# Performance work log

Measured on AMD Instinct MI355X. Metric: run time of the kernel, lower is better.

The kernel has to match this reference:

```python
import jax, jax.numpy as jnp
import numpy as np

C, W, H = 16, 48, 48
OUTDIMS = 4000
COMPONENTS = 1
BATCH = 128
EPS = 1e-6
INIT_NOISE = 1e-3


def setup_inputs() -> dict:
    key = jax.random.key(0)
    kx, kw, kh, kf = jax.random.split(key, 4)
    x = jax.random.normal(kx, (BATCH, C, W, H), dtype=jnp.float32)
    width = jax.random.normal(kw, (OUTDIMS, 1, W, 1, COMPONENTS), dtype=jnp.float32) * INIT_NOISE
    height = jax.random.normal(kh, (OUTDIMS, 1, 1, H, COMPONENTS), dtype=jnp.float32) * INIT_NOISE
    features = jax.random.normal(kf, (OUTDIMS, C, 1, 1), dtype=jnp.float32) * INIT_NOISE
    bias = jnp.zeros((OUTDIMS,), dtype=jnp.float32)
    return {"x": x, "width": width, "height": height, "features": features, "bias": bias}


def reference(x, width, height, features, bias):
    # normalize width over the w axis (dim 2), height over the h axis (dim 3)
    wn = width / jnp.sqrt(jnp.sum(width * width, axis=2, keepdims=True) + EPS)
    hn = height / jnp.sqrt(jnp.sum(height * height, axis=3, keepdims=True) + EPS)
    # spatial mask: sum of outer products over components -> (outdims, w, h)
    spatial = jnp.sum(wn * hn, axis=4)[:, 0]  # broadcast (n,1,w,1,k)*(n,1,1,h,k)
    feat = features[:, :, 0, 0]  # (outdims, c)
    # y[b,n] = sum_{c,w,h} x[b,c,w,h] * spatial[n,w,h] * feat[n,c]  (same math as
    # x.view(N,-1) @ weight.t() where weight = spatial * features, flattened cwh)
    y = jnp.einsum('bcwh,nwh,nc->bn', x, spatial, feat)
    return y + bias[None, :]
```

## Files before the change

kernel.cpp:

```cpp
#include <hip/hip_runtime.h>
#include <stdint.h>

#define OUTD 4000
#define NPAD 4096
#define CC 16
#define WW 48
#define HH 48
#define BB 128
#define KD 768
#define MD 6144
#define EPSF 1e-6f

#define BM 192
#define BNB 256
#define BKU 64
#define UNITS 12
#define AELEMS (BM * BKU)
#define BELEMS (BNB * BKU)
#define SLOTE (AELEMS + BELEMS)
#define THREADS 512
#define XPB 2304

using short8 = __attribute__((ext_vector_type(8))) short;
using f32x4  = __attribute__((ext_vector_type(4))) float;

static __device__ __forceinline__ unsigned short f2bf(float f) {
  union { float f; unsigned int u; } v; v.f = f;
  unsigned int u = v.u;
  unsigned int r = (u + 0x7FFFu + ((u >> 16) & 1u)) >> 16;
  return (unsigned short)r;
}

__global__ __launch_bounds__(256)
void prep_all(const float* __restrict__ x,
              const float* __restrict__ width,
              const float* __restrict__ height,
              const float* __restrict__ feat,
              unsigned short* __restrict__ A,
              unsigned short* __restrict__ Qt,
              float* __restrict__ wnT) {
  __shared__ float smw[4][WW];
  int bid = blockIdx.x;
  if (bid < XPB) {
    int t = bid * 256 + threadIdx.x;
    int e = t * 8;
    int h0 = e % HH;
    int w = (e / HH) % WW;
    int c = (e / (HH * WW)) % CC;
    int b = e / (HH * WW * CC);
    float4 v0 = *(const float4*)(x + e);
    float4 v1 = *(const float4*)(x + e + 4);
    short8 o;
    o[0] = (short)f2bf(v0.x); o[1] = (short)f2bf(v0.y);
    o[2] = (short)f2bf(v0.z); o[3] = (short)f2bf(v0.w);
    o[4] = (short)f2bf(v1.x); o[5] = (short)f2bf(v1.y);
    o[6] = (short)f2bf(v1.z); o[7] = (short)f2bf(v1.w);
    *(short8*)&A[(size_t)(b * WW + w) * KD + c * HH + h0] = o;
  } else {
    int lane = threadIdx.x & 63;
    int wv = threadIdx.x >> 6;
    int nbase = (bid - XPB) * 4;
    int n = nbase + wv;
    bool valid = (n < OUTD);
    float hv = (valid && lane < HH) ? height[n * HH + lane] : 0.f;
    float wvv = (valid && lane < WW) ? width[n * WW + lane] : 0.f;
    float hs = hv * hv, wsum = wvv * wvv;
    #pragma unroll
    for (int off = 32; off > 0; off >>= 1) {
      hs += __shfl_xor(hs, off);
      wsum += __shfl_xor(wsum, off);
    }
    float hnorm = rsqrtf(hs + EPSF);
    float wnorm = rsqrtf(wsum + EPSF);
    if (lane < WW) smw[wv][lane] = wvv * wnorm;
    if (valid) {
      #pragma unroll
      for (int i = lane; i < KD; i += 64) {
        int c = i / HH, h = i % HH;
        Qt[(size_t)n * KD + i] = f2bf(feat[n * CC + c] * height[n * HH + h] * hnorm);
      }
    } else {
      #pragma unroll
      for (int i = lane; i < KD; i += 64) Qt[(size_t)n * KD + i] = 0;
    }
    __syncthreads();
    if (threadIdx.x < WW) {
      int w = threadIdx.x;
      float4 o = make_float4(smw[0][w], smw[1][w], smw[2][w], smw[3][w]);
      *(float4*)&wnT[w * NPAD + nbase] = o;
    }
  }
}

__global__ __launch_bounds__(THREADS, 2)
void gemm_main(const unsigned short* __restrict__ A,
               const unsigned short* __restrict__ Qt,
               const float* __restrict__ wnT,
               const float* __restrict__ bias,
               float* __restrict__ out) {
  __shared__ unsigned short S[2 * SLOTE];

  int tid = threadIdx.x;
  int lane = tid & 63;
  int wid = tid >> 6;
  int wm = wid >> 2;
  int wn = wid & 3;

  int bid = blockIdx.x;
  int xcd = bid & 7;
  int i = bid >> 3;
  int by = xcd * 4 + (i & 3);
  int bxg = i >> 2;
  int n0 = bxg * BNB;
  int m0 = by * BM;

  int rsub = lane >> 3;
  int cg = lane & 7;
  int gsw = (cg ^ rsub) * 8;
  const unsigned short* gA[3];
  const unsigned short* gB[4];
  #pragma unroll
  for (int j = 0; j < 3; ++j)
    gA[j] = A + (size_t)(m0 + (wid * 3 + j) * 8 + rsub) * KD + gsw;
  #pragma unroll
  for (int j = 0; j < 4; ++j)
    gB[j] = Qt + (size_t)(n0 + (wid * 4 + j) * 8 + rsub) * KD + gsw;
  int aD[3], bD[4];
  #pragma unroll
  for (int j = 0; j < 3; ++j) aD[j] = (wid * 3 + j) * 512;
  #pragma unroll
  for (int j = 0; j < 4; ++j) bD[j] = AELEMS + (wid * 4 + j) * 512;

#define SLOTB(u) (((u) & 1) * SLOTE)
#define STAGE(u)                                                                    \
  { _Pragma("unroll")                                                               \
    for (int j = 0; j < 3; ++j)                                                     \
      __builtin_amdgcn_global_load_lds(                                             \
          (const __attribute__((address_space(1))) void*)(gA[j] + (u) * BKU),       \
          (__attribute__((address_space(3))) void*)(&S[SLOTB(u) + aD[j]]), 16, 0, 0); \
    _Pragma("unroll")                                                               \
    for (int j = 0; j < 4; ++j)                                                     \
      __builtin_amdgcn_global_load_lds(                                             \
          (const __attribute__((address_space(1))) void*)(gB[j] + (u) * BKU),       \
          (__attribute__((address_space(3))) void*)(&S[SLOTB(u) + bD[j]]), 16, 0, 0); }

  int q16 = lane & 15;
  int hi = lane >> 4;
  int q7 = q16 & 7;
  int kg0 = ((0 * 4 + hi) ^ q7) * 8;
  int kg1 = ((1 * 4 + hi) ^ q7) * 8;
  int arow = (wm * 96 + q16) * BKU;
  int brow = AELEMS + (wn * 64 + q16) * BKU;

  f32x4 acc[6][4] = {};
  short8 afA[6], bfA[4], afB[6], bfB[4];

#define DSREAD_H(afX, bfX, u, kg)                                      \
  { const unsigned short* sb = &S[SLOTB(u)];                           \
    _Pragma("unroll")                                                  \
    for (int mi = 0; mi < 6; ++mi)                                     \
      afX[mi] = *(const short8*)&sb[arow + mi * 16 * BKU + (kg)];      \
    _Pragma("unroll")                                                  \
    for (int ni = 0; ni < 4; ++ni)                                     \
      bfX[ni] = *(const short8*)&sb[brow + ni * 16 * BKU + (kg)]; }

#define MFMA24(afX, bfX)                                               \
  { _Pragma("unroll")                                                  \
    for (int ni = 0; ni < 4; ++ni)                                     \
      _Pragma("unroll")                                                \
      for (int mi = 0; mi < 6; ++mi)                                   \
        acc[mi][ni] = __builtin_amdgcn_mfma_f32_16x16x32_bf16(afX[mi], bfX[ni], acc[mi][ni], 0, 0, 0); }

  STAGE(0);

  #pragma unroll
  for (int u = 0; u < UNITS; ++u) {
    if (u + 1 < UNITS) {
      STAGE(u + 1);
      asm volatile("s_waitcnt vmcnt(7)" ::: "memory");
    } else {
      asm volatile("s_waitcnt vmcnt(0)" ::: "memory");
    }
    __builtin_amdgcn_s_barrier();
    __builtin_amdgcn_sched_barrier(0);

    DSREAD_H(afA, bfA, u, kg0);
    asm volatile("s_waitcnt lgkmcnt(0)" ::: "memory");
    __builtin_amdgcn_sched_barrier(0);
    DSREAD_H(afB, bfB, u, kg1);
    __builtin_amdgcn_s_setprio(1);
    MFMA24(afA, bfA);
    asm volatile("s_waitcnt lgkmcnt(0)" ::: "memory");
    __builtin_amdgcn_sched_barrier(0);
    MFMA24(afB, bfB);
    __builtin_amdgcn_s_setprio(0);
    __builtin_amdgcn_sched_barrier(0);
  }

  int b0 = by * 4 + wm * 2;
  #pragma unroll
  for (int ni = 0; ni < 4; ++ni) {
    int ng = n0 + wn * 64 + ni * 16 + q16;
    float s0 = 0.f, s1 = 0.f;
    #pragma unroll
    for (int mi = 0; mi < 3; ++mi) {
      int wbase = mi * 16 + hi * 4;
      f32x4 va = acc[mi][ni];
      f32x4 vb = acc[mi + 3][ni];
      #pragma unroll
      for (int r = 0; r < 4; ++r) {
        float t = wnT[(wbase + r) * NPAD + ng];
        s0 += t * va[r];
        s1 += t * vb[r];
      }
    }
    s0 += __shfl_xor(s0, 16); s0 += __shfl_xor(s0, 32);
    s1 += __shfl_xor(s1, 16); s1 += __shfl_xor(s1, 32);
    if (hi == 0 && ng < OUTD) {
      float bv = bias[ng];
      out[(size_t)b0 * OUTD + ng] = s0 + bv;
      out[(size_t)(b0 + 1) * OUTD + ng] = s1 + bv;
    }
  }
#undef STAGE
#undef SLOTB
#undef DSREAD_H
#undef MFMA24
}

extern "C" void kernel_launch(void* const* d_in, const int* in_sizes, int n_in,
                              void* d_out, int out_size, void* d_ws, size_t ws_size,
                              hipStream_t stream) {
  const float* x      = (const float*)d_in[0];
  const float* width  = (const float*)d_in[1];
  const float* height = (const float*)d_in[2];
  const float* feat   = (const float*)d_in[3];
  const float* bias   = (const float*)d_in[4];
  float* out = (float*)d_out;

  char* ws = (char*)d_ws;
  unsigned short* A  = (unsigned short*)ws;
  unsigned short* Qt = (unsigned short*)(ws + 9437184);
  float* wnT         = (float*)(ws + 9437184 + 6291456);

  prep_all<<<dim3(XPB + NPAD / 4), dim3(256), 0, stream>>>(x, width, height, feat, A, Qt, wnT);
  gemm_main<<<dim3(512), dim3(THREADS), 0, stream>>>(A, Qt, wnT, bias, out);
}
```

Before: 48.90 us.

## Use 4 waves with larger per-wave N tile and halve K step

New measurement: 54.68 us. +11.8%, slower.

```diff
diff --git a/kernel.cpp b/kernel.cpp
--- a/kernel.cpp
+++ b/kernel.cpp
@@ -13,12 +13,11 @@
 
 #define BM 192
 #define BNB 256
-#define BKU 64
-#define UNITS 12
+#define BKU 32
+#define UNITS 24
 #define AELEMS (BM * BKU)
-#define BELEMS (BNB * BKU)
-#define SLOTE (AELEMS + BELEMS)
-#define THREADS 512
+#define SLOT_ELEMS ((BM + BNB) * BKU)
+#define THREADS 256
 #define XPB 2304
 
 using short8 = __attribute__((ext_vector_type(8))) short;
@@ -98,13 +97,13 @@
                const float* __restrict__ wnT,
                const float* __restrict__ bias,
                float* __restrict__ out) {
-  __shared__ unsigned short S[2 * SLOTE];
+  __shared__ unsigned short S[2 * SLOT_ELEMS];
 
   int tid = threadIdx.x;
   int lane = tid & 63;
   int wid = tid >> 6;
-  int wm = wid >> 2;
-  int wn = wid & 3;
+  int wm = wid >> 1;
+  int wn = wid & 1;
 
   int bid = blockIdx.x;
   int xcd = bid & 7;
@@ -114,62 +113,41 @@
   int n0 = bxg * BNB;
   int m0 = by * BM;
 
-  int rsub = lane >> 3;
-  int cg = lane & 7;
-  int gsw = (cg ^ rsub) * 8;
-  const unsigned short* gA[3];
-  const unsigned short* gB[4];
-  #pragma unroll
-  for (int j = 0; j < 3; ++j)
-    gA[j] = A + (size_t)(m0 + (wid * 3 + j) * 8 + rsub) * KD + gsw;
-  #pragma unroll
-  for (int j = 0; j < 4; ++j)
-    gB[j] = Qt + (size_t)(n0 + (wid * 4 + j) * 8 + rsub) * KD + gsw;
-  int aD[3], bD[4];
-  #pragma unroll
-  for (int j = 0; j < 3; ++j) aD[j] = (wid * 3 + j) * 512;
-  #pragma unroll
-  for (int j = 0; j < 4; ++j) bD[j] = AELEMS + (wid * 4 + j) * 512;
-
-#define SLOTB(u) (((u) & 1) * SLOTE)
-#define STAGE(u)                                                                    \
-  { _Pragma("unroll")                                                               \
-    for (int j = 0; j < 3; ++j)                                                     \
-      __builtin_amdgcn_global_load_lds(                                             \
-          (const __attribute__((address_space(1))) void*)(gA[j] + (u) * BKU),       \
-          (__attribute__((address_space(3))) void*)(&S[SLOTB(u) + aD[j]]), 16, 0, 0); \
-    _Pragma("unroll")                                                               \
-    for (int j = 0; j < 4; ++j)                                                     \
-      __builtin_amdgcn_global_load_lds(                                             \
-          (const __attribute__((address_space(1))) void*)(gB[j] + (u) * BKU),       \
-          (__attribute__((address_space(3))) void*)(&S[SLOTB(u) + bD[j]]), 16, 0, 0); }
+  int lrow = lane >> 2;
+  int g = lane & 3;
+  int gsw = (g ^ ((lrow >> 1) & 3)) * 8;
+  const unsigned short* gsrc[7];
+  int ldst[7];
+  #pragma unroll
+  for (int j = 0; j < 3; ++j) {
+    int c = wid * 3 + j;
+    gsrc[j] = A + (size_t)(m0 + c * 16 + lrow) * KD + gsw;
+    ldst[j] = c * 512;
+  }
+  #pragma unroll
+  for (int j = 0; j < 4; ++j) {
+    int c = wid * 4 + j;
+    gsrc[3 + j] = Qt + (size_t)(n0 + c * 16 + lrow) * KD + gsw;
+    ldst[3 + j] = AELEMS + c * 512;
+  }
+
+#define SLOTB(u) (((u) & 1) * SLOT_ELEMS)
+#define STAGE(u)                                                                  \
+  { _Pragma("unroll")                                                             \
+    for (int j = 0; j < 7; ++j)                                                   \
+      __builtin_amdgcn_global_load_lds(                                           \
+          (const __attribute__((address_space(1))) void*)(gsrc[j] + (u) * BKU),   \
+          (__attribute__((address_space(3))) void*)(&S[SLOTB(u) + ldst[j]]), 16, 0, 0); }
 
   int q16 = lane & 15;
   int hi = lane >> 4;
-  int q7 = q16 & 7;
-  int kg0 = ((0 * 4 + hi) ^ q7) * 8;
-  int kg1 = ((1 * 4 + hi) ^ q7) * 8;
-  int arow = (wm * 96 + q16) * BKU;
-  int brow = AELEMS + (wn * 64 + q16) * BKU;
-
-  f32x4 acc[6][4] = {};
-  short8 afA[6], bfA[4], afB[6], bfB[4];
-
-#define DSREAD_H(afX, bfX, u, kg)                                      \
-  { const unsigned short* sb = &S[SLOTB(u)];                           \
-    _Pragma("unroll")                                                  \
-    for (int mi = 0; mi < 6; ++mi)                                     \
-      afX[mi] = *(const short8*)&sb[arow + mi * 16 * BKU + (kg)];      \
-    _Pragma("unroll")                                                  \
-    for (int ni = 0; ni < 4; ++ni)                                     \
-      bfX[ni] = *(const short8*)&sb[brow + ni * 16 * BKU + (kg)]; }
-
-#define MFMA24(afX, bfX)                                               \
-  { _Pragma("unroll")                                                  \
-    for (int ni = 0; ni < 4; ++ni)                                     \
-      _Pragma("unroll")                                                \
-      for (int mi = 0; mi < 6; ++mi)                                   \
-        acc[mi][ni] = __builtin_amdgcn_mfma_f32_16x16x32_bf16(afX[mi], bfX[ni], acc[mi][ni], 0, 0, 0); }
+  int kgr = (hi ^ ((q16 >> 1) & 3)) * 8;
+  int arow = (wm * 96 + q16) * BKU + kgr;
+  int brow = AELEMS + (wn * 128 + q16) * BKU + kgr;
+
+  f32x4 acc[6][8] = {};
+  short8 af[6];
+  short8 bf[4];
 
   STAGE(0);
 
@@ -184,23 +162,41 @@
     __builtin_amdgcn_s_barrier();
     __builtin_amdgcn_sched_barrier(0);
 
-    DSREAD_H(afA, bfA, u, kg0);
+    const unsigned short* sb = &S[SLOTB(u)];
+    #pragma unroll
+    for (int mi = 0; mi < 6; ++mi)
+      af[mi] = *(const short8*)&sb[arow + mi * 512];
+    #pragma unroll
+    for (int ni = 0; ni < 4; ++ni)
+      bf[ni] = *(const short8*)&sb[brow + ni * 512];
     asm volatile("s_waitcnt lgkmcnt(0)" ::: "memory");
     __builtin_amdgcn_sched_barrier(0);
-    DSREAD_H(afB, bfB, u, kg1);
     __builtin_amdgcn_s_setprio(1);
-    MFMA24(afA, bfA);
+    #pragma unroll
+    for (int ni = 0; ni < 4; ++ni)
+      #pragma unroll
+      for (int mi = 0; mi < 6; ++mi)
+        acc[mi][ni] = __builtin_amdgcn_mfma_f32_16x16x32_bf16(af[mi], bf[ni], acc[mi][ni], 0, 0, 0);
+    __builtin_amdgcn_s_setprio(0);
+    #pragma unroll
+    for (int ni = 0; ni < 4; ++ni)
+      bf[ni] = *(const short8*)&sb[brow + (4 + ni) * 512];
     asm volatile("s_waitcnt lgkmcnt(0)" ::: "memory");
     __builtin_amdgcn_sched_barrier(0);
-    MFMA24(afB, bfB);
+    __builtin_amdgcn_s_setprio(1);
+    #pragma unroll
+    for (int ni = 0; ni < 4; ++ni)
+      #pragma unroll
+      for (int mi = 0; mi < 6; ++mi)
+        acc[mi][4 + ni] = __builtin_amdgcn_mfma_f32_16x16x32_bf16(af[mi], bf[ni], acc[mi][4 + ni], 0, 0, 0);
     __builtin_amdgcn_s_setprio(0);
     __builtin_amdgcn_sched_barrier(0);
   }
 
   int b0 = by * 4 + wm * 2;
   #pragma unroll
-  for (int ni = 0; ni < 4; ++ni) {
-    int ng = n0 + wn * 64 + ni * 16 + q16;
+  for (int ni = 0; ni < 8; ++ni) {
+    int ng = n0 + wn * 128 + ni * 16 + q16;
     float s0 = 0.f, s1 = 0.f;
     #pragma unroll
     for (int mi = 0; mi < 3; ++mi) {
@@ -224,8 +220,6 @@
   }
 #undef STAGE
 #undef SLOTB
-#undef DSREAD_H
-#undef MFMA24
 }
 
 extern "C" void kernel_launch(void* const* d_in, const int* in_sizes, int n_in,
```

## Shrink GEMM N-tile to 192 and add triple-buffered split A/B staging

Applied to the files above, without the earlier changes.

Result: slower. 56.10 us (+14.7%).

```diff
diff --git a/kernel.cpp b/kernel.cpp
--- a/kernel.cpp
+++ b/kernel.cpp
@@ -2,7 +2,7 @@
 #include <stdint.h>
 
 #define OUTD 4000
-#define NPAD 4096
+#define NP2 4224
 #define CC 16
 #define WW 48
 #define HH 48
@@ -12,14 +12,14 @@
 #define EPSF 1e-6f
 
 #define BM 192
-#define BNB 256
+#define BN 192
 #define BKU 64
 #define UNITS 12
 #define AELEMS (BM * BKU)
-#define BELEMS (BNB * BKU)
-#define SLOTE (AELEMS + BELEMS)
+#define SLOT_ELEMS ((BM + BN) * BKU)
 #define THREADS 512
 #define XPB 2304
+#define WPB (NP2 / 4)
 
 using short8 = __attribute__((ext_vector_type(8))) short;
 using f32x4  = __attribute__((ext_vector_type(4))) float;
@@ -87,7 +87,7 @@
     if (threadIdx.x < WW) {
       int w = threadIdx.x;
       float4 o = make_float4(smw[0][w], smw[1][w], smw[2][w], smw[3][w]);
-      *(float4*)&wnT[w * NPAD + nbase] = o;
+      *(float4*)&wnT[w * NP2 + nbase] = o;
     }
   }
 }
@@ -98,7 +98,7 @@
                const float* __restrict__ wnT,
                const float* __restrict__ bias,
                float* __restrict__ out) {
-  __shared__ unsigned short S[2 * SLOTE];
+  __shared__ unsigned short S[3 * SLOT_ELEMS];
 
   int tid = threadIdx.x;
   int lane = tid & 63;
@@ -108,99 +108,107 @@
 
   int bid = blockIdx.x;
   int xcd = bid & 7;
-  int i = bid >> 3;
-  int by = xcd * 4 + (i & 3);
-  int bxg = i >> 2;
-  int n0 = bxg * BNB;
+  int idx = bid >> 3;
+  int by = xcd * 4 + (idx & 3);
+  int bx = idx >> 2;
+  int n0 = bx * BN;
   int m0 = by * BM;
 
   int rsub = lane >> 3;
   int cg = lane & 7;
   int gsw = (cg ^ rsub) * 8;
   const unsigned short* gA[3];
-  const unsigned short* gB[4];
+  const unsigned short* gB[3];
+  int aD[3], bD[3];
   #pragma unroll
-  for (int j = 0; j < 3; ++j)
-    gA[j] = A + (size_t)(m0 + (wid * 3 + j) * 8 + rsub) * KD + gsw;
-  #pragma unroll
-  for (int j = 0; j < 4; ++j)
-    gB[j] = Qt + (size_t)(n0 + (wid * 4 + j) * 8 + rsub) * KD + gsw;
-  int aD[3], bD[4];
-  #pragma unroll
-  for (int j = 0; j < 3; ++j) aD[j] = (wid * 3 + j) * 512;
-  #pragma unroll
-  for (int j = 0; j < 4; ++j) bD[j] = AELEMS + (wid * 4 + j) * 512;
-
-#define SLOTB(u) (((u) & 1) * SLOTE)
-#define STAGE(u)                                                                    \
-  { _Pragma("unroll")                                                               \
-    for (int j = 0; j < 3; ++j)                                                     \
-      __builtin_amdgcn_global_load_lds(                                             \
-          (const __attribute__((address_space(1))) void*)(gA[j] + (u) * BKU),       \
-          (__attribute__((address_space(3))) void*)(&S[SLOTB(u) + aD[j]]), 16, 0, 0); \
-    _Pragma("unroll")                                                               \
-    for (int j = 0; j < 4; ++j)                                                     \
-      __builtin_amdgcn_global_load_lds(                                             \
-          (const __attribute__((address_space(1))) void*)(gB[j] + (u) * BKU),       \
+  for (int j = 0; j < 3; ++j) {
+    int c = wid * 3 + j;
+    gA[j] = A + (size_t)(m0 + c * 8 + rsub) * KD + gsw;
+    gB[j] = Qt + (size_t)(n0 + c * 8 + rsub) * KD + gsw;
+    aD[j] = c * 512;
+    bD[j] = AELEMS + c * 512;
+  }
+
+#define SLOTB(u) (((u) % 3) * SLOT_ELEMS)
+#define STAGE_A(u)                                                                \
+  { _Pragma("unroll")                                                             \
+    for (int j = 0; j < 3; ++j)                                                   \
+      __builtin_amdgcn_global_load_lds(                                           \
+          (const __attribute__((address_space(1))) void*)(gA[j] + (u) * BKU),     \
+          (__attribute__((address_space(3))) void*)(&S[SLOTB(u) + aD[j]]), 16, 0, 0); }
+#define STAGE_B(u)                                                                \
+  { _Pragma("unroll")                                                             \
+    for (int j = 0; j < 3; ++j)                                                   \
+      __builtin_amdgcn_global_load_lds(                                           \
+          (const __attribute__((address_space(1))) void*)(gB[j] + (u) * BKU),     \
           (__attribute__((address_space(3))) void*)(&S[SLOTB(u) + bD[j]]), 16, 0, 0); }
 
   int q16 = lane & 15;
   int hi = lane >> 4;
   int q7 = q16 & 7;
-  int kg0 = ((0 * 4 + hi) ^ q7) * 8;
-  int kg1 = ((1 * 4 + hi) ^ q7) * 8;
   int arow = (wm * 96 + q16) * BKU;
-  int brow = AELEMS + (wn * 64 + q16) * BKU;
-
-  f32x4 acc[6][4] = {};
-  short8 afA[6], bfA[4], afB[6], bfB[4];
-
-#define DSREAD_H(afX, bfX, u, kg)                                      \
-  { const unsigned short* sb = &S[SLOTB(u)];                           \
-    _Pragma("unroll")                                                  \
-    for (int mi = 0; mi < 6; ++mi)                                     \
-      afX[mi] = *(const short8*)&sb[arow + mi * 16 * BKU + (kg)];      \
-    _Pragma("unroll")                                                  \
-    for (int ni = 0; ni < 4; ++ni)                                     \
-      bfX[ni] = *(const short8*)&sb[brow + ni * 16 * BKU + (kg)]; }
-
-#define MFMA24(afX, bfX)                                               \
-  { _Pragma("unroll")                                                  \
-    for (int ni = 0; ni < 4; ++ni)                                     \
-      _Pragma("unroll")                                                \
-      for (int mi = 0; mi < 6; ++mi)                                   \
-        acc[mi][ni] = __builtin_amdgcn_mfma_f32_16x16x32_bf16(afX[mi], bfX[ni], acc[mi][ni], 0, 0, 0); }
-
-  STAGE(0);
+  int brow = AELEMS + (wn * 48 + q16) * BKU;
+
+  f32x4 acc[6][3] = {};
+  short8 af[2][6];
+  short8 bf[2][3];
+
+#define DSREAD(set, u, kh)                                              \
+  { const unsigned short* sb = &S[SLOTB(u)];                            \
+    const int kgx = (((kh) * 4 + hi) ^ q7) * 8;                         \
+    _Pragma("unroll")                                                   \
+    for (int mi = 0; mi < 6; ++mi)                                      \
+      af[set][mi] = *(const short8*)&sb[arow + mi * 1024 + kgx];        \
+    _Pragma("unroll")                                                   \
+    for (int ni = 0; ni < 3; ++ni)                                      \
+      bf[set][ni] = *(const short8*)&sb[brow + ni * 1024 + kgx]; }
+
+#define MFMA18(set)                                                     \
+  { _Pragma("unroll")                                                   \
+    for (int ni = 0; ni < 3; ++ni)                                      \
+      _Pragma("unroll")                                                 \
+      for (int mi = 0; mi < 6; ++mi)                                    \
+        acc[mi][ni] = __builtin_amdgcn_mfma_f32_16x16x32_bf16(af[set][mi], bf[set][ni], acc[mi][ni], 0, 0, 0); }
+
+  STAGE_A(0); STAGE_B(0);
+  STAGE_A(1); STAGE_B(1);
+  asm volatile("s_waitcnt vmcnt(6)" ::: "memory");
+  __builtin_amdgcn_s_barrier();
+  __builtin_amdgcn_sched_barrier(0);
 
   #pragma unroll
   for (int u = 0; u < UNITS; ++u) {
-    if (u + 1 < UNITS) {
-      STAGE(u + 1);
-      asm volatile("s_waitcnt vmcnt(7)" ::: "memory");
-    } else {
-      asm volatile("s_waitcnt vmcnt(0)" ::: "memory");
-    }
-    __builtin_amdgcn_s_barrier();
-    __builtin_amdgcn_sched_barrier(0);
-
-    DSREAD_H(afA, bfA, u, kg0);
+    DSREAD(0, u, 0);
+    __builtin_amdgcn_sched_barrier(0);
+    __builtin_amdgcn_s_barrier();
+    if (u + 2 < UNITS) STAGE_A(u + 2);
     asm volatile("s_waitcnt lgkmcnt(0)" ::: "memory");
     __builtin_amdgcn_sched_barrier(0);
-    DSREAD_H(afB, bfB, u, kg1);
     __builtin_amdgcn_s_setprio(1);
-    MFMA24(afA, bfA);
+    MFMA18(0);
+    __builtin_amdgcn_s_setprio(0);
+    __builtin_amdgcn_sched_barrier(0);
+    __builtin_amdgcn_s_barrier();
+    DSREAD(1, u, 1);
+    __builtin_amdgcn_sched_barrier(0);
+    __builtin_amdgcn_s_barrier();
+    if (u + 2 < UNITS) STAGE_B(u + 2);
     asm volatile("s_waitcnt lgkmcnt(0)" ::: "memory");
     __builtin_amdgcn_sched_barrier(0);
-    MFMA24(afB, bfB);
+    __builtin_amdgcn_s_setprio(1);
+    MFMA18(1);
     __builtin_amdgcn_s_setprio(0);
+    __builtin_amdgcn_sched_barrier(0);
+    if (u + 2 < UNITS)       asm volatile("s_waitcnt vmcnt(6)" ::: "memory");
+    else if (u + 2 == UNITS) asm volatile("s_waitcnt vmcnt(0)" ::: "memory");
+    __builtin_amdgcn_s_barrier();
     __builtin_amdgcn_sched_barrier(0);
   }
 
   int b0 = by * 4 + wm * 2;
   #pragma unroll
-  for (int ni = 0; ni < 4; ++ni) {
-    int ng = n0 + wn * 64 + ni * 16 + q16;
+  for (int ni = 0; ni < 3; ++ni) {
+    int ng = n0 + wn * 48 + ni * 16 + q16;
     float s0 = 0.f, s1 = 0.f;
     #pragma unroll
     for (int mi = 0; mi < 3; ++mi) {
@@ -209,7 +217,7 @@
       f32x4 vb = acc[mi + 3][ni];
       #pragma unroll
       for (int r = 0; r < 4; ++r) {
-        float t = wnT[(wbase + r) * NPAD + ng];
+        float t = wnT[(wbase + r) * NP2 + ng];
         s0 += t * va[r];
         s1 += t * vb[r];
       }
@@ -222,10 +230,11 @@
       out[(size_t)(b0 + 1) * OUTD + ng] = s1 + bv;
     }
   }
-#undef STAGE
+#undef STAGE_A
+#undef STAGE_B
 #undef SLOTB
-#undef DSREAD_H
-#undef MFMA24
+#undef DSREAD
+#undef MFMA18
 }
 
 extern "C" void kernel_launch(void* const* d_in, const int* in_sizes, int n_in,
@@ -241,8 +250,8 @@
   char* ws = (char*)d_ws;
   unsigned short* A  = (unsigned short*)ws;
   unsigned short* Qt = (unsigned short*)(ws + 9437184);
-  float* wnT         = (float*)(ws + 9437184 + 6291456);
-
-  prep_all<<<dim3(XPB + NPAD / 4), dim3(256), 0, stream>>>(x, width, height, feat, A, Qt, wnT);
-  gemm_main<<<dim3(512), dim3(THREADS), 0, stream>>>(A, Qt, wnT, bias, out);
-}
+  float* wnT         = (float*)(ws + 9437184 + 6488064);
+
+  prep_all<<<dim3(XPB + WPB), dim3(256), 0, stream>>>(x, width, height, feat, A, Qt, wnT);
+  gemm_main<<<dim3(704), dim3(THREADS), 0, stream>>>(A, Qt, wnT, bias, out);
+}
```
